# Kernel optimization log

Measured on AMD Instinct MI355X. Metric: run time of the kernel, lower is better.

Reference implementation:

```python
import jax, jax.numpy as jnp
import numpy as np

NUM_HEADS = 16
EPS = 1e-5


def setup_inputs() -> dict:
    key = jax.random.key(0)
    ks = jax.random.split(key, 9)
    B, S, D = 2, 2048, 1024
    s = 1.0 / np.sqrt(D)
    return {
        "x": jax.random.normal(ks[0], (B, S, D), dtype=jnp.float32),
        "Wq": jax.random.uniform(ks[1], (D, D), jnp.float32, -s, s),
        "bq": jax.random.uniform(ks[2], (D,), jnp.float32, -s, s),
        "Wk": jax.random.uniform(ks[3], (D, D), jnp.float32, -s, s),
        "bk": jax.random.uniform(ks[4], (D,), jnp.float32, -s, s),
        "Wv": jax.random.uniform(ks[5], (D, D), jnp.float32, -s, s),
        "bv": jax.random.uniform(ks[6], (D,), jnp.float32, -s, s),
        "Wo": jax.random.uniform(ks[7], (D, D), jnp.float32, -s, s),
        "bo": jax.random.uniform(ks[8], (D,), jnp.float32, -s, s),
    }


def reference(x, Wq, bq, Wk, bk, Wv, bv, Wo, bo):
    B, S, D = x.shape
    H = NUM_HEADS
    hd = D // H
    # projections -> [B, H, S, hd]
    def proj(W, b):
        return (x @ W + b).reshape(B, S, H, hd).transpose(0, 2, 1, 3)
    Q = proj(Wq, bq)
    K = proj(Wk, bk)
    V = proj(Wv, bv)
    scores = jnp.einsum("bhqd,bhkd->bhqk", Q, K) / jnp.sqrt(jnp.float32(hd))
    attn = jax.nn.softmax(scores, axis=-1)  # dropout is identity in eval mode
    out = jnp.einsum("bhqk,bhkd->bhqd", attn, V)
    out = out.transpose(0, 2, 1, 3).reshape(B, S, D)
    out = jax.nn.relu(out @ Wo + bo)
    mu = jnp.mean(out, axis=-1, keepdims=True)
    var = jnp.var(out, axis=-1, keepdims=True)
    return (out - mu) * jax.lax.rsqrt(var + EPS)
```

## Files before the change

kernel.cpp:

```cpp
#include <hip/hip_runtime.h>
#include <hip/hip_bf16.h>
#include <math.h>

#define Bb 2
#define Ss 2048
#define Dd 1024
#define Hh 16
#define HD 64
#define Mm (Bb*Ss)

typedef __attribute__((ext_vector_type(8))) short bf8_t;
typedef __attribute__((ext_vector_type(4))) float f4_t;
typedef __attribute__((ext_vector_type(4))) unsigned u4_t;
typedef __attribute__((ext_vector_type(2))) unsigned uint2v;

#define LOG2E 1.4426950408889634f

#define AS1 __attribute__((address_space(1)))
#define AS3 __attribute__((address_space(3)))

__device__ __forceinline__ void gl2lds16(const void* g, void* l) {
    __builtin_amdgcn_global_load_lds((const AS1 unsigned int*)g,
                                     (AS3 unsigned int*)l, 16, 0, 0);
}
__device__ __forceinline__ short bfr(float f) {
    __hip_bfloat16 h = __float2bfloat16(f);
    return *reinterpret_cast<short*>(&h);
}
__device__ __forceinline__ unsigned pkbf16(float a, float b) {
    const unsigned ua = __builtin_bit_cast(unsigned, a) + 0x8000u;
    const unsigned ub = __builtin_bit_cast(unsigned, b) + 0x8000u;
    return __builtin_amdgcn_perm(ub, ua, 0x07060302u);
}
__device__ __forceinline__ float fexp2(float x) {
    return __builtin_amdgcn_exp2f(x);
}
__device__ __forceinline__ float b2f(unsigned short u) {
    return __builtin_bit_cast(float, (unsigned)u << 16);
}
__device__ __forceinline__ void pl32(unsigned &a, unsigned &b) {
#if __has_builtin(__builtin_amdgcn_permlane32_swap)
    uint2v r = __builtin_amdgcn_permlane32_swap(a, b, false, false);
    a = r[0]; b = r[1];
#else
    asm volatile("v_permlane32_swap_b32 %0, %1" : "+v"(a), "+v"(b));
#endif
}
__device__ __forceinline__ void pl16(unsigned &a, unsigned &b) {
#if __has_builtin(__builtin_amdgcn_permlane16_swap)
    uint2v r = __builtin_amdgcn_permlane16_swap(a, b, false, false);
    a = r[0]; b = r[1];
#else
    asm volatile("v_permlane16_swap_b32 %0, %1" : "+v"(a), "+v"(b));
#endif
}

__global__ __launch_bounds__(256)
void prep(const float* __restrict__ x,
          const float* __restrict__ w0, const float* __restrict__ w1,
          const float* __restrict__ w2, const float* __restrict__ w3,
          __hip_bfloat16* __restrict__ Wt4, __hip_bfloat16* __restrict__ Xh)
{
    const int z = blockIdx.z;
    if (z < 4) {
        const float* W = (z == 0) ? w0 : (z == 1) ? w1 : (z == 2) ? w2 : w3;
        __hip_bfloat16* Wt = Wt4 + (size_t)z * Dd * Dd;
        __shared__ float t[32][33];
        const int n0 = blockIdx.x * 32, k0 = blockIdx.y * 32;
        const int tx = threadIdx.x & 31, ty = threadIdx.x >> 5;
        #pragma unroll
        for (int rr = 0; rr < 4; ++rr)
            t[ty + rr*8][tx] = W[(size_t)(k0 + ty + rr*8) * Dd + n0 + tx];
        __syncthreads();
        #pragma unroll
        for (int rr = 0; rr < 4; ++rr)
            Wt[(size_t)(n0 + ty + rr*8) * Dd + k0 + tx] =
                __float2bfloat16(t[tx][ty + rr*8]);
    } else {
        const int bid = (z - 4) * 1024 + blockIdx.y * 32 + blockIdx.x;
        const size_t i = ((size_t)bid * 256 + threadIdx.x) * 8;
        const float4 a = *(const float4*)&x[i];
        const float4 b = *(const float4*)&x[i + 4];
        bf8_t o;
        o[0] = bfr(a.x); o[1] = bfr(a.y); o[2] = bfr(a.z); o[3] = bfr(a.w);
        o[4] = bfr(b.x); o[5] = bfr(b.y); o[6] = bfr(b.z); o[7] = bfr(b.w);
        *(bf8_t*)&Xh[i] = o;
    }
}

__global__ __launch_bounds__(256)
void gemm_qkv(const __hip_bfloat16* __restrict__ A,
              const __hip_bfloat16* __restrict__ Bt,
              const float* __restrict__ b0, const float* __restrict__ b1,
              const float* __restrict__ b2,
              __hip_bfloat16* __restrict__ Qh, __hip_bfloat16* __restrict__ Kh,
              __hip_bfloat16* __restrict__ Vt)
{
    __shared__ __align__(16) char pool[34816];
    __hip_bfloat16* As = (__hip_bfloat16*)pool;
    __hip_bfloat16* Bs = As + 2 * 128 * 32;

    const int tid  = threadIdx.x;
    const int wave = tid >> 6;
    const int lane = tid & 63;
    const int llo  = lane & 15;
    const int lhi  = lane >> 4;
    const int wm   = wave & 1;
    const int wn   = wave >> 1;
    const int row0 = blockIdx.y * 128;
    const int col0 = blockIdx.x * 128;

    size_t aoff[2], boff[2];
    int    loff[2];
    #pragma unroll
    for (int p = 0; p < 2; ++p) {
        const int g = p * 256 + wave * 64 + lane;
        const int r = g >> 2;
        const int kc = ((g & 3) ^ ((r >> 1) & 3)) * 8;
        aoff[p] = (size_t)(row0 + r) * Dd + kc;
        boff[p] = (size_t)(col0 + r) * Dd + kc;
        loff[p] = (p * 256 + wave * 64) * 16;
    }
    const __hip_bfloat16* Acur = A;
    const __hip_bfloat16* Bcur = Bt;

    auto stage = [&](int buf) {
        #pragma unroll
        for (int p = 0; p < 2; ++p) {
            gl2lds16(Acur + aoff[p], (char*)As + buf*8192 + loff[p]);
            gl2lds16(Bcur + boff[p], (char*)Bs + buf*8192 + loff[p]);
        }
        Acur += 32; Bcur += 32;
    };

    const int xch = (lhi ^ ((llo >> 1) & 3)) * 8;

    f4_t acc[4][4] = {};
    stage(0);
    for (int kt = 0; kt < 32; ++kt) {
        const int buf = kt & 1;
        __syncthreads();
        if (kt + 1 < 32) stage(buf ^ 1);

        bf8_t a[4], b[4];
        #pragma unroll
        for (int i = 0; i < 4; ++i)
            a[i] = *(const bf8_t*)&As[buf*4096 + (wm*64 + i*16 + llo) * 32 + xch];
        #pragma unroll
        for (int j = 0; j < 4; ++j)
            b[j] = *(const bf8_t*)&Bs[buf*4096 + (wn*64 + j*16 + llo) * 32 + xch];
        #pragma unroll
        for (int i = 0; i < 4; ++i)
            #pragma unroll
            for (int j = 0; j < 4; ++j)
                acc[i][j] = __builtin_amdgcn_mfma_f32_16x16x32_bf16(
                    a[i], b[j], acc[i][j], 0, 0, 0);
    }

    const int sel   = col0 >> 10;
    const int cbase = col0 & 1023;
    __hip_bfloat16* Ls = (__hip_bfloat16*)pool;
    __syncthreads();

    float bv[4];
    const float* bp = (sel == 0) ? b0 : (sel == 1) ? b1 : b2;
    #pragma unroll
    for (int j = 0; j < 4; ++j) bv[j] = bp[cbase + wn*64 + j*16 + llo];
    const float scale = (sel == 0) ? 0.125f * LOG2E : 1.0f;

    if (sel < 2) {
        #pragma unroll
        for (int i = 0; i < 4; ++i)
            #pragma unroll
            for (int r = 0; r < 4; ++r) {
                const int ml = wm*64 + i*16 + lhi*4 + r;
                #pragma unroll
                for (int j = 0; j < 4; ++j)
                    Ls[ml*136 + wn*64 + j*16 + llo] =
                        __float2bfloat16((acc[i][j][r] + bv[j]) * scale);
            }
        __syncthreads();
        __hip_bfloat16* outQK = (sel == 0) ? Qh : Kh;
        #pragma unroll
        for (int p = 0; p < 8; ++p) {
            const int id = p*256 + tid;
            const int rl = id >> 4;
            const int c8 = (id & 15) * 8;
            const bf8_t v = *(const bf8_t*)&Ls[rl*136 + c8];
            const int m  = row0 + rl;
            const int b_ = m >> 11, s_ = m & (Ss - 1);
            const int col = cbase + c8;
            *(bf8_t*)&outQK[((size_t)(b_*Hh + (col >> 6))*Ss + s_)*HD + (col & 63)] = v;
        }
    } else {
        #pragma unroll
        for (int i = 0; i < 4; ++i)
            #pragma unroll
            for (int r = 0; r < 4; ++r) {
                const int ml = wm*64 + i*16 + lhi*4 + r;
                #pragma unroll
                for (int j = 0; j < 4; ++j)
                    Ls[(wn*64 + j*16 + llo)*136 + ml] =
                        __float2bfloat16(acc[i][j][r] + bv[j]);
            }
        __syncthreads();
        const int b_ = row0 >> 11;
        const int sb = row0 & (Ss - 1);
        #pragma unroll
        for (int p = 0; p < 8; ++p) {
            const int cl = p*16 + (tid >> 4);
            const int m  = (tid & 15) * 8;
            const bf8_t v = *(const bf8_t*)&Ls[cl*136 + m];
            const int cc = cbase + cl;
            *(bf8_t*)&Vt[((size_t)(b_*Hh + (cc >> 6))*HD + (cc & 63))*Ss + sb + m] = v;
        }
    }
}

__global__ __launch_bounds__(256, 2)
void attn_mfma(const __hip_bfloat16* __restrict__ Qh,
               const __hip_bfloat16* __restrict__ Kh,
               const __hip_bfloat16* __restrict__ Vt,
               __hip_bfloat16* __restrict__ Ah)
{
    const int b    = blockIdx.z;
    const int h    = blockIdx.y;
    const int wave = threadIdx.x >> 6;
    const int lane = threadIdx.x & 63;
    const int llo  = lane & 15;
    const int lhi  = lane >> 4;
    const int qb   = blockIdx.x * 128 + wave * 32;

    const size_t base = ((size_t)(b*Hh + h)) * Ss * HD;

    __shared__ __hip_bfloat16 Ks[2][2 * 64 * 32];
    __shared__ __hip_bfloat16 Vs[2][2 * 64 * 32];

    int koff[2], voff[2], loff[2];
    #pragma unroll
    for (int it = 0; it < 2; ++it) {
        const int g  = it*256 + wave*64 + lane;
        const int hf = g >> 8;
        const int rr = (g >> 2) & 63;
        const int c8 = ((g & 3) ^ ((rr >> 1) & 3)) * 8;
        koff[it] = rr*HD + hf*32 + c8;
        voff[it] = rr*Ss + hf*32 + c8;
        loff[it] = (it*256 + wave*64) * 16;
    }
    const __hip_bfloat16* Kcur = Kh + base;
    const __hip_bfloat16* Vcur = Vt + base;

    auto stage = [&](int buf) {
        #pragma unroll
        for (int it = 0; it < 2; ++it) {
            gl2lds16(Kcur + koff[it], (char*)&Ks[buf][0] + loff[it]);
            gl2lds16(Vcur + voff[it], (char*)&Vs[buf][0] + loff[it]);
        }
        Kcur += 64 * HD;
        Vcur += 64;
    };

    bf8_t qf[2][2];
    #pragma unroll
    for (int s = 0; s < 2; ++s)
        #pragma unroll
        for (int d = 0; d < 2; ++d)
            qf[s][d] = *(const bf8_t*)&Qh[base + (size_t)(qb + 16*s + llo)*HD + 32*d + lhi*8];

    f4_t o_[2][4];
    float lacc[2];
    #pragma unroll
    for (int s = 0; s < 2; ++s) {
        #pragma unroll
        for (int n = 0; n < 4; ++n) o_[s][n] = (f4_t){0.f,0.f,0.f,0.f};
        lacc[s] = 0.f;
    }

    const f4_t zf = {0.f,0.f,0.f,0.f};
    const int xch = (lhi ^ ((llo >> 1) & 3)) * 8;

    stage(0);

    for (int t = 0; t < Ss/64; ++t) {
        const int buf = t & 1;
        __syncthreads();
        if (t + 1 < Ss/64) stage(buf ^ 1);

        bf8_t kf[4][2];
        #pragma unroll
        for (int kc = 0; kc < 4; ++kc)
            #pragma unroll
            for (int d = 0; d < 2; ++d)
                kf[kc][d] = *(const bf8_t*)&Ks[buf][d*2048 + (kc*16 + llo)*32 + xch];

        f4_t sacc[2][4];
        #pragma unroll
        for (int s = 0; s < 2; ++s)
            #pragma unroll
            for (int kc = 0; kc < 4; ++kc) {
                sacc[s][kc] = __builtin_amdgcn_mfma_f32_16x16x32_bf16(kf[kc][0], qf[s][0], zf, 0, 0, 0);
                sacc[s][kc] = __builtin_amdgcn_mfma_f32_16x16x32_bf16(kf[kc][1], qf[s][1], sacc[s][kc], 0, 0, 0);
            }

        bf8_t vf[4][2];
        #pragma unroll
        for (int nc = 0; nc < 4; ++nc)
            #pragma unroll
            for (int d = 0; d < 2; ++d)
                vf[nc][d] = *(const bf8_t*)&Vs[buf][d*2048 + (nc*16 + llo)*32 + xch];

        bf8_t pf[2][2];
        #pragma unroll
        for (int s = 0; s < 2; ++s) {
            unsigned w[4][2];
            #pragma unroll
            for (int kc = 0; kc < 4; ++kc) {
                const float p0 = fexp2(sacc[s][kc][0]);
                const float p1 = fexp2(sacc[s][kc][1]);
                const float p2 = fexp2(sacc[s][kc][2]);
                const float p3 = fexp2(sacc[s][kc][3]);
                lacc[s] += (p0 + p1) + (p2 + p3);
                w[kc][0] = pkbf16(p0, p1);
                w[kc][1] = pkbf16(p2, p3);
            }
            #pragma unroll
            for (int d = 0; d < 2; ++d) {
                u4_t pu;
                #pragma unroll
                for (int hh = 0; hh < 2; ++hh) {
                    unsigned U = w[2*d][hh], V = w[2*d+1][hh];
                    pl32(U, V);
                    pl16(U, V);
                    pu[hh]     = U;
                    pu[2 + hh] = V;
                }
                pf[s][d] = __builtin_bit_cast(bf8_t, pu);
            }
        }

        #pragma unroll
        for (int d = 0; d < 2; ++d)
            #pragma unroll
            for (int nc = 0; nc < 4; ++nc)
                #pragma unroll
                for (int s = 0; s < 2; ++s)
                    o_[s][nc] = __builtin_amdgcn_mfma_f32_16x16x32_bf16(pf[s][d], vf[nc][d], o_[s][nc], 0, 0, 0);
    }

    #pragma unroll
    for (int s = 0; s < 2; ++s) {
        lacc[s] += __shfl_xor(lacc[s], 16);
        lacc[s] += __shfl_xor(lacc[s], 32);
    }

    #pragma unroll
    for (int s = 0; s < 2; ++s) {
        #pragma unroll
        for (int r = 0; r < 4; ++r) {
            const float lv  = __shfl(lacc[s], 4*lhi + r);
            const float inv = 1.0f / lv;
            const int q = qb + 16*s + 4*lhi + r;
            __hip_bfloat16* orow = &Ah[((size_t)(b*Ss) + q)*Dd + h*HD + llo];
            #pragma unroll
            for (int nc = 0; nc < 4; ++nc)
                orow[16*nc] = __float2bfloat16(o_[s][nc][r] * inv);
        }
    }
}

__global__ __launch_bounds__(256)
void gemm_out(const __hip_bfloat16* __restrict__ A,
              const __hip_bfloat16* __restrict__ Bt,
              __hip_bfloat16* __restrict__ Ro)
{
    __shared__ __hip_bfloat16 As[2][128 * 32];
    __shared__ __hip_bfloat16 Bs[2][128 * 32];

    const int tid  = threadIdx.x;
    const int wave = tid >> 6;
    const int lane = tid & 63;
    const int llo  = lane & 15;
    const int lhi  = lane >> 4;
    const int wm   = wave & 1;
    const int wn   = wave >> 1;
    const int row0 = blockIdx.y * 128;
    const int col0 = blockIdx.x * 128;
    const int z    = blockIdx.z;

    size_t aoff[2], boff[2];
    int    loff[2];
    #pragma unroll
    for (int p = 0; p < 2; ++p) {
        const int g = p * 256 + wave * 64 + lane;
        const int r = g >> 2;
        const int kc = ((g & 3) ^ ((r >> 1) & 3)) * 8;
        aoff[p] = (size_t)(row0 + r) * Dd + kc;
        boff[p] = (size_t)(col0 + r) * Dd + kc;
        loff[p] = (p * 256 + wave * 64) * 16;
    }
    const __hip_bfloat16* Acur = A  + (size_t)z * (Dd/2);
    const __hip_bfloat16* Bcur = Bt + (size_t)z * (Dd/2);

    auto stage = [&](int buf) {
        #pragma unroll
        for (int p = 0; p < 2; ++p) {
            gl2lds16(Acur + aoff[p], (char*)&As[buf][0] + loff[p]);
            gl2lds16(Bcur + boff[p], (char*)&Bs[buf][0] + loff[p]);
        }
        Acur += 32; Bcur += 32;
    };

    const int xch = (lhi ^ ((llo >> 1) & 3)) * 8;

    f4_t acc[4][4] = {};
    stage(0);
    for (int kt = 0; kt < 16; ++kt) {
        const int buf = kt & 1;
        __syncthreads();
        if (kt + 1 < 16) stage(buf ^ 1);

        bf8_t a[4], b[4];
        #pragma unroll
        for (int i = 0; i < 4; ++i)
            a[i] = *(const bf8_t*)&As[buf][(wm*64 + i*16 + llo) * 32 + xch];
        #pragma unroll
        for (int j = 0; j < 4; ++j)
            b[j] = *(const bf8_t*)&Bs[buf][(wn*64 + j*16 + llo) * 32 + xch];
        #pragma unroll
        for (int i = 0; i < 4; ++i)
            #pragma unroll
            for (int j = 0; j < 4; ++j)
                acc[i][j] = __builtin_amdgcn_mfma_f32_16x16x32_bf16(
                    a[i], b[j], acc[i][j], 0, 0, 0);
    }

    __hip_bfloat16* Roz = Ro + (size_t)z * Mm * Dd;
    #pragma unroll
    for (int i = 0; i < 4; ++i) {
        #pragma unroll
        for (int r = 0; r < 4; ++r) {
            const int m = row0 + wm*64 + i*16 + lhi*4 + r;
            #pragma unroll
            for (int j = 0; j < 4; ++j) {
                const int col = col0 + wn*64 + j*16 + llo;
                Roz[(size_t)m * Dd + col] = __float2bfloat16(acc[i][j][r]);
            }
        }
    }
}

__global__ __launch_bounds__(256)
void layernorm(const __hip_bfloat16* __restrict__ P0,
               const __hip_bfloat16* __restrict__ P1,
               const float* __restrict__ bias, float* __restrict__ out)
{
    const int row = blockIdx.x;
    const int c = threadIdx.x;
    const ushort4 a = ((const ushort4*)(P0 + (size_t)row*Dd))[c];
    const ushort4 b = ((const ushort4*)(P1 + (size_t)row*Dd))[c];
    const float4 bb = ((const float4*)bias)[c];
    float4 v;
    v.x = fmaxf(b2f(a.x) + b2f(b.x) + bb.x, 0.0f);
    v.y = fmaxf(b2f(a.y) + b2f(b.y) + bb.y, 0.0f);
    v.z = fmaxf(b2f(a.z) + b2f(b.z) + bb.z, 0.0f);
    v.w = fmaxf(b2f(a.w) + b2f(b.w) + bb.w, 0.0f);

    float s  = v.x + v.y + v.z + v.w;
    float ss = v.x*v.x + v.y*v.y + v.z*v.z + v.w*v.w;
    #pragma unroll
    for (int off = 32; off > 0; off >>= 1) {
        s  += __shfl_down(s,  off);
        ss += __shfl_down(ss, off);
    }
    __shared__ float rs[4], rss[4];
    const int wid = c >> 6, lid = c & 63;
    if (lid == 0) { rs[wid] = s; rss[wid] = ss; }
    __syncthreads();
    s  = rs[0] + rs[1] + rs[2] + rs[3];
    ss = rss[0] + rss[1] + rss[2] + rss[3];
    const float mean = s * (1.0f / Dd);
    const float var  = ss * (1.0f / Dd) - mean * mean;
    const float rstd = rsqrtf(var + 1e-5f);
    float4 o;
    o.x = (v.x - mean) * rstd;
    o.y = (v.y - mean) * rstd;
    o.z = (v.z - mean) * rstd;
    o.w = (v.w - mean) * rstd;
    ((float4*)(out + (size_t)row*Dd))[c] = o;
}

extern "C" void kernel_launch(void* const* d_in, const int* in_sizes, int n_in,
                              void* d_out, int out_size, void* d_ws, size_t ws_size,
                              hipStream_t stream)
{
    const float* x  = (const float*)d_in[0];
    const float* Wq = (const float*)d_in[1];
    const float* bq = (const float*)d_in[2];
    const float* Wk = (const float*)d_in[3];
    const float* bk = (const float*)d_in[4];
    const float* Wv = (const float*)d_in[5];
    const float* bv = (const float*)d_in[6];
    const float* Wo = (const float*)d_in[7];
    const float* bo = (const float*)d_in[8];
    float* out = (float*)d_out;

    __hip_bfloat16* Xh    = (__hip_bfloat16*)d_ws;
    __hip_bfloat16* Wqkvt = Xh    + (size_t)Mm*Dd;
    __hip_bfloat16* Wot   = Wqkvt + (size_t)3*Dd*Dd;
    __hip_bfloat16* Ah    = Wot   + (size_t)Dd*Dd;
    __hip_bfloat16* Qh    = Ah    + (size_t)Mm*Dd;
    __hip_bfloat16* Kh    = Qh    + (size_t)Mm*Dd;
    __hip_bfloat16* Vt    = Kh    + (size_t)Mm*Dd;
    __hip_bfloat16* Rb    = Qh;

    prep<<<dim3(32, 32, 6), dim3(256), 0, stream>>>(x, Wq, Wk, Wv, Wo, Wqkvt, Xh);
    gemm_qkv<<<dim3(3*Dd/128, Mm/128), dim3(256), 0, stream>>>(
        Xh, Wqkvt, bq, bk, bv, Qh, Kh, Vt);
    attn_mfma<<<dim3(Ss/128, Hh, Bb), dim3(256), 0, stream>>>(Qh, Kh, Vt, Ah);
    gemm_out<<<dim3(Dd/128, Mm/128, 2), dim3(256), 0, stream>>>(Ah, Wot, Rb);
    layernorm<<<dim3(Mm), dim3(256), 0, stream>>>(Rb, Rb + (size_t)Mm*Dd, bo, out);
}
```

Measured before the change: 198.6 us.

## Remap block IDs for XCD-local L2 reuse and compute softmax row sums via MFMA

Remaps linear block indices in the QKV GEMM, attention and output GEMM kernels so that blocks dispatched round-robin to the same XCD work on neighbouring tiles or the same heads. The aim is to improve L2 reuse of shared A/B tiles and K/V data. It also replaces the per-lane scalar accumulation of softmax denominators, and the shuffles that followed, with an extra MFMA against a ones vector. That puts the row sum directly into the output layout, at the cost of four additional MFMAs per tile and a sum taken over bf16-rounded probabilities.

```diff
diff --git a/kernel.cpp b/kernel.cpp
--- a/kernel.cpp
+++ b/kernel.cpp
@@ -100,6 +100,11 @@
     __hip_bfloat16* As = (__hip_bfloat16*)pool;
     __hip_bfloat16* Bs = As + 2 * 128 * 32;
 
+    const int lin  = blockIdx.y * 24 + blockIdx.x;
+    const int nlin = (lin & 7) * 96 + (lin >> 3);
+    const int bx   = nlin % 24;
+    const int by   = nlin / 24;
+
     const int tid  = threadIdx.x;
     const int wave = tid >> 6;
     const int lane = tid & 63;
@@ -107,8 +112,8 @@
     const int lhi  = lane >> 4;
     const int wm   = wave & 1;
     const int wn   = wave >> 1;
-    const int row0 = blockIdx.y * 128;
-    const int col0 = blockIdx.x * 128;
+    const int row0 = by * 128;
+    const int col0 = bx * 128;
 
     size_t aoff[2], boff[2];
     int    loff[2];
@@ -223,13 +228,19 @@
                const __hip_bfloat16* __restrict__ Vt,
                __hip_bfloat16* __restrict__ Ah)
 {
-    const int b    = blockIdx.z;
-    const int h    = blockIdx.y;
+    const int lin  = (blockIdx.z * Hh + blockIdx.y) * (Ss/128) + blockIdx.x;
+    const int xcd  = lin & 7;
+    const int slot = lin >> 3;
+    const int grp  = (xcd << 2) | (slot >> 4);
+    const int qc   = slot & 15;
+    const int b    = grp >> 4;
+    const int h    = grp & 15;
+
     const int wave = threadIdx.x >> 6;
     const int lane = threadIdx.x & 63;
     const int llo  = lane & 15;
     const int lhi  = lane >> 4;
-    const int qb   = blockIdx.x * 128 + wave * 32;
+    const int qb   = qc * 128 + wave * 32;
 
     const size_t base = ((size_t)(b*Hh + h)) * Ss * HD;
 
@@ -268,13 +279,15 @@
             qf[s][d] = *(const bf8_t*)&Qh[base + (size_t)(qb + 16*s + llo)*HD + 32*d + lhi*8];
 
     f4_t o_[2][4];
-    float lacc[2];
+    f4_t lsum[2];
     #pragma unroll
     for (int s = 0; s < 2; ++s) {
         #pragma unroll
         for (int n = 0; n < 4; ++n) o_[s][n] = (f4_t){0.f,0.f,0.f,0.f};
-        lacc[s] = 0.f;
-    }
+        lsum[s] = (f4_t){0.f,0.f,0.f,0.f};
+    }
+    const short oneb = 0x3F80;
+    const bf8_t vones = {oneb,oneb,oneb,oneb,oneb,oneb,oneb,oneb};
 
     const f4_t zf = {0.f,0.f,0.f,0.f};
     const int xch = (lhi ^ ((llo >> 1) & 3)) * 8;
@@ -319,7 +332,6 @@
                 const float p1 = fexp2(sacc[s][kc][1]);
                 const float p2 = fexp2(sacc[s][kc][2]);
                 const float p3 = fexp2(sacc[s][kc][3]);
-                lacc[s] += (p0 + p1) + (p2 + p3);
                 w[kc][0] = pkbf16(p0, p1);
                 w[kc][1] = pkbf16(p2, p3);
             }
@@ -339,6 +351,12 @@
         }
 
         #pragma unroll
+        for (int s = 0; s < 2; ++s)
+            #pragma unroll
+            for (int d = 0; d < 2; ++d)
+                lsum[s] = __builtin_amdgcn_mfma_f32_16x16x32_bf16(pf[s][d], vones, lsum[s], 0, 0, 0);
+
+        #pragma unroll
         for (int d = 0; d < 2; ++d)
             #pragma unroll
             for (int nc = 0; nc < 4; ++nc)
@@ -349,16 +367,9 @@
 
     #pragma unroll
     for (int s = 0; s < 2; ++s) {
-        lacc[s] += __shfl_xor(lacc[s], 16);
-        lacc[s] += __shfl_xor(lacc[s], 32);
-    }
-
-    #pragma unroll
-    for (int s = 0; s < 2; ++s) {
         #pragma unroll
         for (int r = 0; r < 4; ++r) {
-            const float lv  = __shfl(lacc[s], 4*lhi + r);
-            const float inv = 1.0f / lv;
+            const float inv = 1.0f / lsum[s][r];
             const int q = qb + 16*s + 4*lhi + r;
             __hip_bfloat16* orow = &Ah[((size_t)(b*Ss) + q)*Dd + h*HD + llo];
             #pragma unroll
@@ -376,6 +387,13 @@
     __shared__ __hip_bfloat16 As[2][128 * 32];
     __shared__ __hip_bfloat16 Bs[2][128 * 32];
 
+    const int lin  = (blockIdx.z * 32 + blockIdx.y) * 8 + blockIdx.x;
+    const int nlin = (lin & 7) * 64 + (lin >> 3);
+    const int bx   = nlin & 7;
+    const int rest = nlin >> 3;
+    const int by   = rest & 31;
+    const int z    = rest >> 5;
+
     const int tid  = threadIdx.x;
     const int wave = tid >> 6;
     const int lane = tid & 63;
@@ -383,9 +401,8 @@
     const int lhi  = lane >> 4;
     const int wm   = wave & 1;
     const int wn   = wave >> 1;
-    const int row0 = blockIdx.y * 128;
-    const int col0 = blockIdx.x * 128;
-    const int z    = blockIdx.z;
+    const int row0 = by * 128;
+    const int col0 = bx * 128;
 
     size_t aoff[2], boff[2];
     int    loff[2];
```

Result: faster. 191.7 us (-3.5%).
